# Performance work log

Measured on AMD Instinct MI355X. Metric: run time of the kernel, lower is better.

## Reference

```python
import jax, jax.numpy as jnp
import numpy as np

B, S, D, H, DK, HID = 2, 2048, 768, 12, 64, 3072
EPS = 1e-5

def layernorm(x, g, b):
    mu = jnp.mean(x, axis=-1, keepdims=True)
    var = jnp.var(x, axis=-1, keepdims=True)
    return (x - mu) * jax.lax.rsqrt(var + EPS) * g + b

def setup_inputs() -> dict:
    key = jax.random.key(0)
    ks = jax.random.split(key, 9)
    std = 0.02
    x = jax.random.normal(ks[0], (B, S, D), dtype=jnp.float32)
    Wq = jax.random.normal(ks[1], (H, D, DK), dtype=jnp.float32) * std
    Wk = jax.random.normal(ks[2], (H, D, DK), dtype=jnp.float32) * std
    Wv = jax.random.normal(ks[3], (H, D, DK), dtype=jnp.float32) * std
    Wo = jax.random.normal(ks[4], (H * DK, D), dtype=jnp.float32) * std
    W1 = jax.random.normal(ks[5], (D, HID), dtype=jnp.float32) * std
    b1 = jnp.zeros((HID,), dtype=jnp.float32)
    W2 = jax.random.normal(ks[6], (HID, D), dtype=jnp.float32) * std
    b2 = jnp.zeros((D,), dtype=jnp.float32)
    g_ln1 = jnp.ones((D,), dtype=jnp.float32)
    b_ln1 = jnp.zeros((D,), dtype=jnp.float32)
    g_ln2 = jnp.ones((D,), dtype=jnp.float32)
    b_ln2 = jnp.zeros((D,), dtype=jnp.float32)
    return {"x": x, "Wq": Wq, "Wk": Wk, "Wv": Wv, "Wo": Wo,
            "W1": W1, "b1": b1, "W2": W2, "b2": b2,
            "g_ln1": g_ln1, "b_ln1": b_ln1, "g_ln2": g_ln2, "b_ln2": b_ln2}

def reference(x, Wq, Wk, Wv, Wo, W1, b1, W2, b2, g_ln1, b_ln1, g_ln2, b_ln2):
    seq = x.shape[1]
    h = layernorm(x, g_ln1, b_ln1)
    # per-head projections, vectorized over heads: [B,H,S,DK]
    Q = jnp.einsum('bsd,hdk->bhsk', h, Wq)
    K = jnp.einsum('bsd,hdk->bhsk', h, Wk)
    V = jnp.einsum('bsd,hdk->bhsk', h, Wv)
    scores = jnp.einsum('bhsk,bhtk->bhst', Q, K) / jnp.sqrt(jnp.float32(DK))
    mask = jnp.triu(jnp.full((seq, seq), -jnp.inf, dtype=scores.dtype), k=1)
    A = jax.nn.softmax(scores + mask, axis=-1)
    out = jnp.einsum('bhst,bhtk->bhsk', A, V)  # [B,H,S,DK]
    # concat heads (matches torch.cat over heads dim=-1)
    out = out.transpose(0, 2, 1, 3).reshape(x.shape[0], seq, H * DK)
    attn = out @ Wo
    y = x + attn
    h2 = layernorm(y, g_ln2, b_ln2)
    mlp = jax.nn.gelu(h2 @ W1 + b1, approximate=False) @ W2 + b2
    return y + mlp
```

## Files before the change

kernel.cpp:

```cpp
#include <hip/hip_runtime.h>
#include <hip/hip_bf16.h>
#include <cstdint>
#include <cstddef>

using bf16 = __hip_bfloat16;
typedef __attribute__((ext_vector_type(8))) short short8;
typedef __attribute__((ext_vector_type(4))) float f32x4;
typedef __attribute__((ext_vector_type(2))) int i32x2;

#define DEV static __device__ __forceinline__

#define MROWS 4096
#define SEQ   2048
#define DMODEL 768
#define NHEAD 12
#define DHEAD 64
#define HID   3072
#define QSCALE 0.1803368801111204f

DEV void gload16(const void* g, void* l) {
  __builtin_amdgcn_global_load_lds((const __attribute__((address_space(1))) void*)g,
                                   (__attribute__((address_space(3))) void*)l, 16, 0, 0);
}

template <int CTRL>
DEV float dppf(float x) {
  return __builtin_bit_cast(float,
      __builtin_amdgcn_mov_dpp(__builtin_bit_cast(int, x), CTRL, 0xF, 0xF, true));
}
DEV float red_add16(float x) {
  x += dppf<0xB1>(x);
  x += dppf<0x4E>(x);
  x += dppf<0x141>(x);
  x += dppf<0x140>(x);
  return x;
}

DEV float gelu_exact(float x) {
  float z = fabsf(x) * 0.70710678118f;
  float t = __builtin_amdgcn_rcpf(fmaf(0.3275911f, z, 1.0f));
  float poly = fmaf(1.061405429f, t, -1.453152027f);
  poly = fmaf(poly, t, 1.421413741f);
  poly = fmaf(poly, t, -0.284496736f);
  poly = fmaf(poly, t, 0.254829592f);
  poly *= t;
  float e = __builtin_amdgcn_exp2f(-0.72134752044f * x * x);
  float erfv = fmaf(-poly, e, 1.0f);
  erfv = copysignf(erfv, x);
  return 0.5f * x * (1.0f + erfv);
}

__global__ __launch_bounds__(256) void cvt_qkv_k(const float* __restrict__ Wq,
                                                 const float* __restrict__ Wk,
                                                 const float* __restrict__ Wv,
                                                 bf16* __restrict__ out) {
  int idx = blockIdx.x * 256 + threadIdx.x;
  int n = idx / DMODEL, d = idx - n * DMODEL;
  int proj = n / DMODEL;
  int within = n - proj * DMODEL;
  int hh = within >> 6, k = within & 63;
  const float* W = (proj == 0) ? Wq : (proj == 1 ? Wk : Wv);
  out[idx] = __float2bfloat16(W[((size_t)hh * DMODEL + d) * DHEAD + k]);
}

__global__ __launch_bounds__(256) void cvt_t_k(const float* __restrict__ W,
                                               bf16* __restrict__ out, int R, int C) {
  int idx = blockIdx.x * 256 + threadIdx.x;
  int c = idx / R, r = idx - c * R;
  out[idx] = __float2bfloat16(W[(size_t)r * C + c]);
}

__global__ __launch_bounds__(256) void ln_k(const float* __restrict__ in,
                                            const float* __restrict__ gam,
                                            const float* __restrict__ bet,
                                            bf16* __restrict__ out) {
  int r = blockIdx.x;
  int tid = threadIdx.x;
  const float* p = in + (size_t)r * DMODEL;
  float v0 = p[tid], v1 = p[tid + 256], v2 = p[tid + 512];
  float s = v0 + v1 + v2;
  float ss = v0 * v0 + v1 * v1 + v2 * v2;
#pragma unroll
  for (int off = 1; off < 64; off <<= 1) {
    s += __shfl_xor(s, off);
    ss += __shfl_xor(ss, off);
  }
  __shared__ float rs[4], rss[4];
  int w = tid >> 6, l = tid & 63;
  if (l == 0) { rs[w] = s; rss[w] = ss; }
  __syncthreads();
  s = rs[0] + rs[1] + rs[2] + rs[3];
  ss = rss[0] + rss[1] + rss[2] + rss[3];
  float mean = s * (1.0f / 768.0f);
  float var = ss * (1.0f / 768.0f) - mean * mean;
  float inv = rsqrtf(var + 1e-5f);
  bf16* o = out + (size_t)r * DMODEL;
  o[tid]       = __float2bfloat16((v0 - mean) * inv * gam[tid] + bet[tid]);
  o[tid + 256] = __float2bfloat16((v1 - mean) * inv * gam[tid + 256] + bet[tid + 256]);
  o[tid + 512] = __float2bfloat16((v2 - mean) * inv * gam[tid + 512] + bet[tid + 512]);
}

template <int EPI>
DEV void gemm_epilogue(int r, int c, float v,
                       bf16* __restrict__ ob, float* __restrict__ of,
                       const float* __restrict__ add, const float* __restrict__ bias,
                       bf16* __restrict__ vt) {
  if constexpr (EPI == 0) {
    if (c < 1536) {
      float scv = (c < DMODEL) ? QSCALE : 1.0f;
      ob[(size_t)r * 1536 + c] = __float2bfloat16(v * scv);
    } else {
      int within = c - 1536;
      int hh = within >> 6, kk = within & 63;
      int bidx = r >> 11, sq = r & 2047;
      int sqp = (sq & ~63) | ((sq & 15) << 2) | ((sq >> 4) & 3);
      vt[(((size_t)bidx * NHEAD + hh) * DHEAD + kk) * SEQ + sqp] = __float2bfloat16(v);
    }
  } else if constexpr (EPI == 1) {
    of[(size_t)r * DMODEL + c] = add[(size_t)r * DMODEL + c] + v;
  } else if constexpr (EPI == 2) {
    ob[(size_t)r * HID + c] = __float2bfloat16(gelu_exact(v + bias[c]));
  } else {
    of[(size_t)r * DMODEL + c] = add[(size_t)r * DMODEL + c] + v + bias[c];
  }
}

template <int EPI, int BM, int BN>
__global__ __launch_bounds__(256) void gemm_bt(const bf16* __restrict__ A,
                                               const bf16* __restrict__ Bt, int K,
                                               bf16* __restrict__ ob,
                                               float* __restrict__ of,
                                               const float* __restrict__ add,
                                               const float* __restrict__ bias,
                                               bf16* __restrict__ vt) {
  __shared__ bf16 sA[2][BM * 32];
  __shared__ bf16 sB[2][BN * 32];
  constexpr int MI = BM / 32;
  constexpr int NI = BN / 32;
  constexpr int LOADS = (BM == 128 ? 2 : 1) + (BN == 128 ? 2 : 1);
  const int tid = threadIdx.x;
  const int w = tid >> 6, l = tid & 63;
  const int lr = l & 15, lg = l >> 4;
  const int mbase = blockIdx.y * BM, nbase = blockIdx.x * BN;
  const int wm = (w >> 1) * (BM / 2), wn = (w & 1) * (BN / 2);

  f32x4 acc[MI][NI];
#pragma unroll
  for (int i = 0; i < MI; ++i)
#pragma unroll
    for (int j = 0; j < NI; ++j) acc[i][j] = (f32x4)0.0f;

  const int srow = l >> 2;
  const int scol = ((l & 3) ^ ((l >> 3) & 3)) * 8;
  const bf16* gA = A + (size_t)(mbase + (BM == 128 ? w * 32 : w * 16) + srow) * K + scol;
  const bf16* gB = Bt + (size_t)(nbase + (BN == 128 ? w * 32 : w * 16) + srow) * K + scol;
  const int foff = (lg ^ ((lr >> 1) & 3)) * 8;

#define GSTAGE(bufi, t)                                                      \
  {                                                                          \
    const int k0_ = (t) * 32;                                                \
    if constexpr (BM == 128) {                                               \
      gload16(gA + k0_, &sA[bufi][w * 1024]);                                \
      gload16(gA + k0_ + (size_t)16 * K, &sA[bufi][w * 1024 + 512]);         \
    } else {                                                                 \
      gload16(gA + k0_, &sA[bufi][w * 512]);                                 \
    }                                                                        \
    if constexpr (BN == 128) {                                               \
      gload16(gB + k0_, &sB[bufi][w * 1024]);                                \
      gload16(gB + k0_ + (size_t)16 * K, &sB[bufi][w * 1024 + 512]);         \
    } else {                                                                 \
      gload16(gB + k0_, &sB[bufi][w * 512]);                                 \
    }                                                                        \
  }

  const int nt = K >> 5;
  GSTAGE(0, 0);
  for (int t = 0; t < nt; ++t) {
    const int cur = t & 1;
    if (t + 1 < nt) {
      GSTAGE(cur ^ 1, t + 1);
      if constexpr (LOADS == 4)      asm volatile("s_waitcnt vmcnt(4)" ::: "memory");
      else if constexpr (LOADS == 3) asm volatile("s_waitcnt vmcnt(3)" ::: "memory");
      else                           asm volatile("s_waitcnt vmcnt(2)" ::: "memory");
    } else {
      asm volatile("s_waitcnt vmcnt(0)" ::: "memory");
    }
    __builtin_amdgcn_s_barrier();

    short8 a[MI], bb[NI];
#pragma unroll
    for (int mi = 0; mi < MI; ++mi)
      a[mi] = *(const short8*)&sA[cur][(wm + mi * 16 + lr) * 32 + foff];
#pragma unroll
    for (int ni = 0; ni < NI; ++ni)
      bb[ni] = *(const short8*)&sB[cur][(wn + ni * 16 + lr) * 32 + foff];
#pragma unroll
    for (int mi = 0; mi < MI; ++mi)
#pragma unroll
      for (int ni = 0; ni < NI; ++ni)
        acc[mi][ni] = __builtin_amdgcn_mfma_f32_16x16x32_bf16(a[mi], bb[ni], acc[mi][ni], 0, 0, 0);

    __builtin_amdgcn_s_barrier();
  }
#undef GSTAGE

  const int row0 = mbase + wm + lg * 4;
  const int col0 = nbase + wn + lr;
#pragma unroll
  for (int mi = 0; mi < MI; ++mi)
#pragma unroll
    for (int ni = 0; ni < NI; ++ni)
#pragma unroll
      for (int i = 0; i < 4; ++i)
        gemm_epilogue<EPI>(row0 + mi * 16 + i, col0 + ni * 16, acc[mi][ni][i],
                           ob, of, add, bias, vt);
}

template <int EPI>
__global__ __launch_bounds__(256) void gemm64_bt(const bf16* __restrict__ A,
                                                 const bf16* __restrict__ Bt, int K,
                                                 bf16* __restrict__ ob,
                                                 float* __restrict__ of,
                                                 const float* __restrict__ add,
                                                 const float* __restrict__ bias) {
  __shared__ bf16 sA[2][64 * 64];
  __shared__ bf16 sB[2][64 * 64];
  const int tid = threadIdx.x;
  const int w = tid >> 6, l = tid & 63;
  const int lr = l & 15, lg = l >> 4;
  const int mbase = blockIdx.y * 64, nbase = blockIdx.x * 64;
  const int wm = (w >> 1) * 32, wn = (w & 1) * 32;

  f32x4 acc[2][2];
#pragma unroll
  for (int i = 0; i < 2; ++i)
#pragma unroll
    for (int j = 0; j < 2; ++j) acc[i][j] = (f32x4)0.0f;

  const int srow3 = l >> 3;
  const int csrc = ((l & 7) ^ srow3) * 8;
  const bf16* gA = A + (size_t)(mbase + w * 16 + srow3) * K + csrc;
  const bf16* gB = Bt + (size_t)(nbase + w * 16 + srow3) * K + csrc;

  int rowa[2], rowb[2], cswz[2];
#pragma unroll
  for (int mi = 0; mi < 2; ++mi) rowa[mi] = (wm + mi * 16 + lr) * 64;
#pragma unroll
  for (int ni = 0; ni < 2; ++ni) rowb[ni] = (wn + ni * 16 + lr) * 64;
#pragma unroll
  for (int kk = 0; kk < 2; ++kk) cswz[kk] = (((kk * 4 + lg) ^ (lr & 7)) << 3);

#define GSTAGE64(bufi, t)                                                    \
  {                                                                          \
    const int k0_ = (t) * 64;                                                \
    gload16(gA + k0_,                 &sA[bufi][(w * 16) * 64]);             \
    gload16(gA + k0_ + (size_t)8 * K, &sA[bufi][(w * 16 + 8) * 64]);         \
    gload16(gB + k0_,                 &sB[bufi][(w * 16) * 64]);             \
    gload16(gB + k0_ + (size_t)8 * K, &sB[bufi][(w * 16 + 8) * 64]);         \
  }

  const int nt = K >> 6;
  GSTAGE64(0, 0);
  for (int t = 0; t < nt; ++t) {
    const int cur = t & 1;
    if (t + 1 < nt) {
      GSTAGE64(cur ^ 1, t + 1);
      asm volatile("s_waitcnt vmcnt(4)" ::: "memory");
    } else {
      asm volatile("s_waitcnt vmcnt(0)" ::: "memory");
    }
    __builtin_amdgcn_s_barrier();

    short8 a[2][2], bb[2][2];
#pragma unroll
    for (int mi = 0; mi < 2; ++mi)
#pragma unroll
      for (int kk = 0; kk < 2; ++kk)
        a[mi][kk] = *(const short8*)&sA[cur][rowa[mi] + cswz[kk]];
#pragma unroll
    for (int ni = 0; ni < 2; ++ni)
#pragma unroll
      for (int kk = 0; kk < 2; ++kk)
        bb[ni][kk] = *(const short8*)&sB[cur][rowb[ni] + cswz[kk]];
#pragma unroll
    for (int mi = 0; mi < 2; ++mi)
#pragma unroll
      for (int ni = 0; ni < 2; ++ni) {
        acc[mi][ni] = __builtin_amdgcn_mfma_f32_16x16x32_bf16(a[mi][0], bb[ni][0], acc[mi][ni], 0, 0, 0);
        acc[mi][ni] = __builtin_amdgcn_mfma_f32_16x16x32_bf16(a[mi][1], bb[ni][1], acc[mi][ni], 0, 0, 0);
      }

    __builtin_amdgcn_s_barrier();
  }
#undef GSTAGE64

  const int row0 = mbase + wm + lg * 4;
  const int col0 = nbase + wn + lr;
#pragma unroll
  for (int mi = 0; mi < 2; ++mi)
#pragma unroll
    for (int ni = 0; ni < 2; ++ni)
#pragma unroll
      for (int i = 0; i < 4; ++i)
        gemm_epilogue<EPI>(row0 + mi * 16 + i, col0 + ni * 16, acc[mi][ni][i],
                           ob, of, add, bias, nullptr);
}

__global__ __launch_bounds__(256) void attn_k(const bf16* __restrict__ qk,
                                              const bf16* __restrict__ vt,
                                              bf16* __restrict__ o,
                                              float* __restrict__ opart,
                                              float* __restrict__ lpart) {
  __shared__ bf16 sK[2][64 * 64];
  __shared__ bf16 sV[2][64 * 64];
  __shared__ bf16 sP[64 * 64];

  const int d = blockIdx.x;
  const int bh = d % 24;
  const int rank = d / 24;
  const int j = 79 - rank;
  int qt, chunk, nch;
  if (j < 8)       { qt = j;                        chunk = 0;           nch = 1; }
  else if (j < 24) { int r_ = j - 8;  qt = 8  + (r_ >> 1); chunk = r_ & 1;  nch = 2; }
  else if (j < 48) { int r_ = j - 24; qt = 16 + r_ / 3;    chunk = r_ % 3;  nch = 3; }
  else             { int r_ = j - 48; qt = 24 + (r_ >> 2); chunk = r_ & 3;  nch = 4; }
  const int nt_q = qt + 1;
  const int t0 = (chunk * nt_q) / nch;
  const int t1 = ((chunk + 1) * nt_q) / nch;

  const int b = bh / NHEAD, h = bh - b * NHEAD;
  const int qbase = qt * 64;
  const int tid = threadIdx.x, w = tid >> 6, l = tid & 63;
  const int lr = l & 15, lg = l >> 4;

  short8 q[2];
#pragma unroll
  for (int kk = 0; kk < 2; ++kk)
    q[kk] = *(const short8*)&qk[(size_t)(b * SEQ + qbase + w * 16 + lr) * 1536 + h * DHEAD + kk * 32 + lg * 8];

  f32x4 oa[4];
  float lst[4];
#pragma unroll
  for (int i = 0; i < 4; ++i) { oa[i] = (f32x4)0.0f; lst[i] = 0.0f; }

  const int srow3 = l >> 3;
  const int csrc = (l & 7) ^ srow3;
  const bf16* gKb = qk + ((size_t)(b * SEQ) + w * 16 + srow3) * 1536 + DMODEL + h * DHEAD + csrc * 8;
  const bf16* gVb = vt + ((size_t)bh * DHEAD + w * 16 + srow3) * SEQ + csrc * 8;

  int rowb[4], cswz[2];
#pragma unroll
  for (int ni = 0; ni < 4; ++ni) rowb[ni] = (ni * 16 + lr) * 64;
#pragma unroll
  for (int kk = 0; kk < 2; ++kk) cswz[kk] = (((kk * 4 + lg) ^ (lr & 7)) << 3);
  const int prow = (w * 16 + lr) * 64;

#define STAGE(buf, t)                                                              \
  {                                                                                \
    const int kb_ = (t) * 64;                                                      \
    gload16(gKb + (size_t)kb_ * 1536,        &sK[buf][(w * 16) * 64]);             \
    gload16(gKb + (size_t)(kb_ + 8) * 1536,  &sK[buf][(w * 16 + 8) * 64]);         \
    gload16(gVb + kb_,                       &sV[buf][(w * 16) * 64]);             \
    gload16(gVb + kb_ + (size_t)8 * SEQ,     &sV[buf][(w * 16 + 8) * 64]);         \
  }

  STAGE(0, t0);

  for (int t = t0; t < t1; ++t) {
    const int cur = (t - t0) & 1;
    const int kb = t * 64;
    if (t + 1 < t1) {
      STAGE(cur ^ 1, t + 1);
      asm volatile("s_waitcnt vmcnt(4)" ::: "memory");
    } else {
      asm volatile("s_waitcnt vmcnt(0)" ::: "memory");
    }
    __builtin_amdgcn_s_barrier();

    const bf16* sKc = sK[cur];
    const bf16* sVc = sV[cur];

    f32x4 sc[4];
    __builtin_amdgcn_s_setprio(1);
#pragma unroll
    for (int ni = 0; ni < 4; ++ni) {
      sc[ni] = (f32x4)0.0f;
#pragma unroll
      for (int kk = 0; kk < 2; ++kk) {
        short8 kf = *(const short8*)&sKc[rowb[ni] + cswz[kk]];
        sc[ni] = __builtin_amdgcn_mfma_f32_16x16x32_bf16(q[kk], kf, sc[ni], 0, 0, 0);
      }
    }
    __builtin_amdgcn_s_setprio(0);

    const bool need_mask = (kb + 63) > (qbase + w * 16);
    const int qrow0 = qbase + w * 16 + lg * 4;
#pragma unroll
    for (int i = 0; i < 4; ++i) {
      float v0 = sc[0][i], v1 = sc[1][i], v2 = sc[2][i], v3 = sc[3][i];
      if (need_mask) {
        const int qg = qrow0 + i;
        v0 = (kb + lr      > qg) ? -1e30f : v0;
        v1 = (kb + 16 + lr > qg) ? -1e30f : v1;
        v2 = (kb + 32 + lr > qg) ? -1e30f : v2;
        v3 = (kb + 48 + lr > qg) ? -1e30f : v3;
      }
      float p0 = exp2f(v0), p1 = exp2f(v1), p2 = exp2f(v2), p3 = exp2f(v3);
      lst[i] += (p0 + p1) + (p2 + p3);
      int r0, r1;
      asm("v_cvt_pk_bf16_f32 %0, %1, %2" : "=v"(r0) : "v"(p0), "v"(p1));
      asm("v_cvt_pk_bf16_f32 %0, %1, %2" : "=v"(r1) : "v"(p2), "v"(p3));
      const int rrow = w * 16 + lg * 4 + i;
      *(i32x2*)((char*)sP + rrow * 128 + ((lr * 8) ^ ((rrow & 7) << 4))) = (i32x2){r0, r1};
    }

    short8 pf0 = *(const short8*)&sP[prow + cswz[0]];
    short8 pf1 = *(const short8*)&sP[prow + cswz[1]];
    __builtin_amdgcn_s_setprio(1);
#pragma unroll
    for (int nk = 0; nk < 4; ++nk) {
      short8 vf0 = *(const short8*)&sVc[rowb[nk] + cswz[0]];
      short8 vf1 = *(const short8*)&sVc[rowb[nk] + cswz[1]];
      oa[nk] = __builtin_amdgcn_mfma_f32_16x16x32_bf16(pf0, vf0, oa[nk], 0, 0, 0);
      oa[nk] = __builtin_amdgcn_mfma_f32_16x16x32_bf16(pf1, vf1, oa[nk], 0, 0, 0);
    }
    __builtin_amdgcn_s_setprio(0);
    __builtin_amdgcn_s_barrier();
  }
#undef STAGE

#pragma unroll
  for (int i = 0; i < 4; ++i) lst[i] = red_add16(lst[i]);

  if (nch == 1) {
#pragma unroll
    for (int i = 0; i < 4; ++i) {
      const float rl = __builtin_amdgcn_rcpf(lst[i]);
#pragma unroll
      for (int nk = 0; nk < 4; ++nk) {
        int row = qbase + w * 16 + lg * 4 + i;
        int col = h * DHEAD + nk * 16 + lr;
        o[(size_t)(b * SEQ + row) * DMODEL + col] = __float2bfloat16(oa[nk][i] * rl);
      }
    }
  } else {
    const int slot = bh * 80 + j;
    float* op = opart + (size_t)slot * 4096;
#pragma unroll
    for (int i = 0; i < 4; ++i) {
      const int row = w * 16 + lg * 4 + i;
#pragma unroll
      for (int nk = 0; nk < 4; ++nk)
        op[row * 64 + nk * 16 + lr] = oa[nk][i];
      if (lr == 0) lpart[slot * 64 + row] = lst[i];
    }
  }
}

__global__ __launch_bounds__(256) void attn_comb_k(const float* __restrict__ opart,
                                                   const float* __restrict__ lpart,
                                                   bf16* __restrict__ o) {
  const int s = blockIdx.x;
  const int bh = s / 24;
  const int qt = 8 + (s - bh * 24);
  const int b = bh / NHEAD, h = bh - b * NHEAD;
  const int bb = qt >> 3;
  const int nch = bb + 1;
  const int S0 = 4 * bb * (bb + 1) + (qt - 8 * bb) * (bb + 1);
  const int slot0 = bh * 80 + S0;

  const int tid = threadIdx.x;
  const int row = tid >> 2;
  const int c0 = (tid & 3) * 16;

  f32x4 acc[4];
#pragma unroll
  for (int e = 0; e < 4; ++e) acc[e] = (f32x4)0.0f;
  float lsum = 0.0f;
  for (int c = 0; c < nch; ++c) {
    const f32x4* op = (const f32x4*)(opart + (size_t)(slot0 + c) * 4096 + row * 64 + c0);
    lsum += lpart[(slot0 + c) * 64 + row];
#pragma unroll
    for (int e = 0; e < 4; ++e) acc[e] += op[e];
  }
  const float rl = 1.0f / lsum;
  bf16* po = o + (size_t)(b * SEQ + qt * 64 + row) * DMODEL + h * DHEAD + c0;
#pragma unroll
  for (int e = 0; e < 4; ++e)
#pragma unroll
    for (int k = 0; k < 4; ++k)
      po[e * 4 + k] = __float2bfloat16(acc[e][k] * rl);
}

extern "C" void kernel_launch(void* const* d_in, const int* in_sizes, int n_in,
                              void* d_out, int out_size, void* d_ws, size_t ws_size,
                              hipStream_t stream) {
  (void)in_sizes; (void)n_in; (void)out_size; (void)ws_size;
  const float* x   = (const float*)d_in[0];
  const float* Wq  = (const float*)d_in[1];
  const float* Wk  = (const float*)d_in[2];
  const float* Wv  = (const float*)d_in[3];
  const float* Wo  = (const float*)d_in[4];
  const float* W1  = (const float*)d_in[5];
  const float* b1  = (const float*)d_in[6];
  const float* W2  = (const float*)d_in[7];
  const float* b2  = (const float*)d_in[8];
  const float* g1  = (const float*)d_in[9];
  const float* be1 = (const float*)d_in[10];
  const float* g2  = (const float*)d_in[11];
  const float* be2 = (const float*)d_in[12];
  float* out = (float*)d_out;

  char* p = (char*)d_ws;
  bf16* WqkvT = (bf16*)p; p += (size_t)2304 * 768 * 2;
  bf16* WoT   = (bf16*)p; p += (size_t)768 * 768 * 2;
  bf16* W1T   = (bf16*)p; p += (size_t)3072 * 768 * 2;
  bf16* W2T   = (bf16*)p; p += (size_t)768 * 3072 * 2;
  bf16* h1    = (bf16*)p; p += (size_t)MROWS * DMODEL * 2;
  char* alias0 = p;
  bf16* QK    = (bf16*)p; p += (size_t)MROWS * 1536 * 2;
  bf16* Vt    = (bf16*)p; p += (size_t)24 * DHEAD * SEQ * 2;
  bf16* O     = (bf16*)p; p += (size_t)MROWS * DMODEL * 2;
  float* y    = (float*)p; p += (size_t)MROWS * DMODEL * 4;
  bf16* h2    = (bf16*)p; p += (size_t)MROWS * DMODEL * 2;
  float* Opart = (float*)p; p += (size_t)24 * 80 * 4096 * 4;
  float* Lpart = (float*)p; p += (size_t)24 * 80 * 64 * 4;
  bf16* U     = (bf16*)alias0;

  dim3 blk(256);
  cvt_qkv_k<<<(2304 * 768) / 256, blk, 0, stream>>>(Wq, Wk, Wv, WqkvT);
  cvt_t_k<<<(768 * 768) / 256, blk, 0, stream>>>(Wo, WoT, 768, 768);
  cvt_t_k<<<(768 * 3072) / 256, blk, 0, stream>>>(W1, W1T, 768, 3072);
  cvt_t_k<<<(3072 * 768) / 256, blk, 0, stream>>>(W2, W2T, 3072, 768);
  ln_k<<<MROWS, blk, 0, stream>>>(x, g1, be1, h1);
  gemm_bt<0, 128, 128><<<dim3(18, 32), blk, 0, stream>>>(h1, WqkvT, 768, QK, nullptr, nullptr, nullptr, Vt);
  attn_k<<<1920, blk, 0, stream>>>(QK, Vt, O, Opart, Lpart);
  attn_comb_k<<<576, blk, 0, stream>>>(Opart, Lpart, O);
  gemm64_bt<1><<<dim3(12, 64), blk, 0, stream>>>(O, WoT, 768, nullptr, y, x, nullptr);
  ln_k<<<MROWS, blk, 0, stream>>>(y, g2, be2, h2);
  gemm64_bt<2><<<dim3(48, 64), blk, 0, stream>>>(h2, W1T, 768, U, nullptr, nullptr, b1);
  gemm64_bt<3><<<dim3(12, 64), blk, 0, stream>>>(U, W2T, 3072, nullptr, out, y, b2);
}
```

Baseline: 218.8 us.

## Use LDS-tiled transpose for weight conversion and 64x64 GEMM for QKV

Replaces the naive strided-read weight transpose-and-convert kernels with 64x64 shared-memory tiled transposes. Both the reads and the bf16 writes become coalesced. The QKV projection moves from the 128x128 GEMM to the 64x64 K-step-64 GEMM, giving 2304 blocks instead of 576 for better CU occupancy. The cost is less operand reuse per block in the QKV GEMM.

```diff
diff --git a/kernel.cpp b/kernel.cpp
--- a/kernel.cpp
+++ b/kernel.cpp
@@ -50,24 +50,46 @@
   return 0.5f * x * (1.0f + erfv);
 }
 
-__global__ __launch_bounds__(256) void cvt_qkv_k(const float* __restrict__ Wq,
-                                                 const float* __restrict__ Wk,
-                                                 const float* __restrict__ Wv,
-                                                 bf16* __restrict__ out) {
-  int idx = blockIdx.x * 256 + threadIdx.x;
-  int n = idx / DMODEL, d = idx - n * DMODEL;
-  int proj = n / DMODEL;
-  int within = n - proj * DMODEL;
-  int hh = within >> 6, k = within & 63;
-  const float* W = (proj == 0) ? Wq : (proj == 1 ? Wk : Wv);
-  out[idx] = __float2bfloat16(W[((size_t)hh * DMODEL + d) * DHEAD + k]);
-}
-
-__global__ __launch_bounds__(256) void cvt_t_k(const float* __restrict__ W,
-                                               bf16* __restrict__ out, int R, int C) {
-  int idx = blockIdx.x * 256 + threadIdx.x;
-  int c = idx / R, r = idx - c * R;
-  out[idx] = __float2bfloat16(W[(size_t)r * C + c]);
+__global__ __launch_bounds__(256) void tcvt_k(const float* __restrict__ in,
+                                              bf16* __restrict__ out, int R, int C) {
+  __shared__ float tile[64][65];
+  const int r0 = blockIdx.y * 64, c0 = blockIdx.x * 64;
+  const int tid = threadIdx.x, lr = tid & 63, lw = tid >> 6;
+#pragma unroll
+  for (int i = 0; i < 16; ++i) {
+    int r = i * 4 + lw;
+    tile[r][lr] = in[(size_t)(r0 + r) * C + c0 + lr];
+  }
+  __syncthreads();
+#pragma unroll
+  for (int i = 0; i < 16; ++i) {
+    int c = i * 4 + lw;
+    out[(size_t)(c0 + c) * R + r0 + lr] = __float2bfloat16(tile[lr][c]);
+  }
+}
+
+__global__ __launch_bounds__(256) void tcvt_qkv_k(const float* __restrict__ Wq,
+                                                  const float* __restrict__ Wk,
+                                                  const float* __restrict__ Wv,
+                                                  bf16* __restrict__ out) {
+  __shared__ float tile[64][65];
+  const int z = blockIdx.z;
+  const int proj = z / 12, hh = z - proj * 12;
+  const float* W = (proj == 0 ? Wq : (proj == 1 ? Wk : Wv)) + (size_t)hh * DMODEL * DHEAD;
+  bf16* o = out + (size_t)(proj * DMODEL + hh * DHEAD) * DMODEL;
+  const int r0 = blockIdx.y * 64;
+  const int tid = threadIdx.x, lr = tid & 63, lw = tid >> 6;
+#pragma unroll
+  for (int i = 0; i < 16; ++i) {
+    int r = i * 4 + lw;
+    tile[r][lr] = W[(size_t)(r0 + r) * DHEAD + lr];
+  }
+  __syncthreads();
+#pragma unroll
+  for (int i = 0; i < 16; ++i) {
+    int c = i * 4 + lw;
+    o[(size_t)c * DMODEL + r0 + lr] = __float2bfloat16(tile[lr][c]);
+  }
 }
 
 __global__ __launch_bounds__(256) void ln_k(const float* __restrict__ in,
@@ -125,104 +147,14 @@
   }
 }
 
-template <int EPI, int BM, int BN>
-__global__ __launch_bounds__(256) void gemm_bt(const bf16* __restrict__ A,
-                                               const bf16* __restrict__ Bt, int K,
-                                               bf16* __restrict__ ob,
-                                               float* __restrict__ of,
-                                               const float* __restrict__ add,
-                                               const float* __restrict__ bias,
-                                               bf16* __restrict__ vt) {
-  __shared__ bf16 sA[2][BM * 32];
-  __shared__ bf16 sB[2][BN * 32];
-  constexpr int MI = BM / 32;
-  constexpr int NI = BN / 32;
-  constexpr int LOADS = (BM == 128 ? 2 : 1) + (BN == 128 ? 2 : 1);
-  const int tid = threadIdx.x;
-  const int w = tid >> 6, l = tid & 63;
-  const int lr = l & 15, lg = l >> 4;
-  const int mbase = blockIdx.y * BM, nbase = blockIdx.x * BN;
-  const int wm = (w >> 1) * (BM / 2), wn = (w & 1) * (BN / 2);
-
-  f32x4 acc[MI][NI];
-#pragma unroll
-  for (int i = 0; i < MI; ++i)
-#pragma unroll
-    for (int j = 0; j < NI; ++j) acc[i][j] = (f32x4)0.0f;
-
-  const int srow = l >> 2;
-  const int scol = ((l & 3) ^ ((l >> 3) & 3)) * 8;
-  const bf16* gA = A + (size_t)(mbase + (BM == 128 ? w * 32 : w * 16) + srow) * K + scol;
-  const bf16* gB = Bt + (size_t)(nbase + (BN == 128 ? w * 32 : w * 16) + srow) * K + scol;
-  const int foff = (lg ^ ((lr >> 1) & 3)) * 8;
-
-#define GSTAGE(bufi, t)                                                      \
-  {                                                                          \
-    const int k0_ = (t) * 32;                                                \
-    if constexpr (BM == 128) {                                               \
-      gload16(gA + k0_, &sA[bufi][w * 1024]);                                \
-      gload16(gA + k0_ + (size_t)16 * K, &sA[bufi][w * 1024 + 512]);         \
-    } else {                                                                 \
-      gload16(gA + k0_, &sA[bufi][w * 512]);                                 \
-    }                                                                        \
-    if constexpr (BN == 128) {                                               \
-      gload16(gB + k0_, &sB[bufi][w * 1024]);                                \
-      gload16(gB + k0_ + (size_t)16 * K, &sB[bufi][w * 1024 + 512]);         \
-    } else {                                                                 \
-      gload16(gB + k0_, &sB[bufi][w * 512]);                                 \
-    }                                                                        \
-  }
-
-  const int nt = K >> 5;
-  GSTAGE(0, 0);
-  for (int t = 0; t < nt; ++t) {
-    const int cur = t & 1;
-    if (t + 1 < nt) {
-      GSTAGE(cur ^ 1, t + 1);
-      if constexpr (LOADS == 4)      asm volatile("s_waitcnt vmcnt(4)" ::: "memory");
-      else if constexpr (LOADS == 3) asm volatile("s_waitcnt vmcnt(3)" ::: "memory");
-      else                           asm volatile("s_waitcnt vmcnt(2)" ::: "memory");
-    } else {
-      asm volatile("s_waitcnt vmcnt(0)" ::: "memory");
-    }
-    __builtin_amdgcn_s_barrier();
-
-    short8 a[MI], bb[NI];
-#pragma unroll
-    for (int mi = 0; mi < MI; ++mi)
-      a[mi] = *(const short8*)&sA[cur][(wm + mi * 16 + lr) * 32 + foff];
-#pragma unroll
-    for (int ni = 0; ni < NI; ++ni)
-      bb[ni] = *(const short8*)&sB[cur][(wn + ni * 16 + lr) * 32 + foff];
-#pragma unroll
-    for (int mi = 0; mi < MI; ++mi)
-#pragma unroll
-      for (int ni = 0; ni < NI; ++ni)
-        acc[mi][ni] = __builtin_amdgcn_mfma_f32_16x16x32_bf16(a[mi], bb[ni], acc[mi][ni], 0, 0, 0);
-
-    __builtin_amdgcn_s_barrier();
-  }
-#undef GSTAGE
-
-  const int row0 = mbase + wm + lg * 4;
-  const int col0 = nbase + wn + lr;
-#pragma unroll
-  for (int mi = 0; mi < MI; ++mi)
-#pragma unroll
-    for (int ni = 0; ni < NI; ++ni)
-#pragma unroll
-      for (int i = 0; i < 4; ++i)
-        gemm_epilogue<EPI>(row0 + mi * 16 + i, col0 + ni * 16, acc[mi][ni][i],
-                           ob, of, add, bias, vt);
-}
-
 template <int EPI>
 __global__ __launch_bounds__(256) void gemm64_bt(const bf16* __restrict__ A,
                                                  const bf16* __restrict__ Bt, int K,
                                                  bf16* __restrict__ ob,
                                                  float* __restrict__ of,
                                                  const float* __restrict__ add,
-                                                 const float* __restrict__ bias) {
+                                                 const float* __restrict__ bias,
+                                                 bf16* __restrict__ vt) {
   __shared__ bf16 sA[2][64 * 64];
   __shared__ bf16 sB[2][64 * 64];
   const int tid = threadIdx.x;
@@ -303,7 +235,7 @@
 #pragma unroll
       for (int i = 0; i < 4; ++i)
         gemm_epilogue<EPI>(row0 + mi * 16 + i, col0 + ni * 16, acc[mi][ni][i],
-                           ob, of, add, bias, nullptr);
+                           ob, of, add, bias, vt);
 }
 
 __global__ __launch_bounds__(256) void attn_k(const bf16* __restrict__ qk,
@@ -528,16 +460,16 @@
   bf16* U     = (bf16*)alias0;
 
   dim3 blk(256);
-  cvt_qkv_k<<<(2304 * 768) / 256, blk, 0, stream>>>(Wq, Wk, Wv, WqkvT);
-  cvt_t_k<<<(768 * 768) / 256, blk, 0, stream>>>(Wo, WoT, 768, 768);
-  cvt_t_k<<<(768 * 3072) / 256, blk, 0, stream>>>(W1, W1T, 768, 3072);
-  cvt_t_k<<<(3072 * 768) / 256, blk, 0, stream>>>(W2, W2T, 3072, 768);
+  tcvt_qkv_k<<<dim3(1, 12, 36), blk, 0, stream>>>(Wq, Wk, Wv, WqkvT);
+  tcvt_k<<<dim3(12, 12), blk, 0, stream>>>(Wo, WoT, 768, 768);
+  tcvt_k<<<dim3(48, 12), blk, 0, stream>>>(W1, W1T, 768, 3072);
+  tcvt_k<<<dim3(12, 48), blk, 0, stream>>>(W2, W2T, 3072, 768);
   ln_k<<<MROWS, blk, 0, stream>>>(x, g1, be1, h1);
-  gemm_bt<0, 128, 128><<<dim3(18, 32), blk, 0, stream>>>(h1, WqkvT, 768, QK, nullptr, nullptr, nullptr, Vt);
+  gemm64_bt<0><<<dim3(36, 64), blk, 0, stream>>>(h1, WqkvT, 768, QK, nullptr, nullptr, nullptr, Vt);
   attn_k<<<1920, blk, 0, stream>>>(QK, Vt, O, Opart, Lpart);
   attn_comb_k<<<576, blk, 0, stream>>>(Opart, Lpart, O);
-  gemm64_bt<1><<<dim3(12, 64), blk, 0, stream>>>(O, WoT, 768, nullptr, y, x, nullptr);
+  gemm64_bt<1><<<dim3(12, 64), blk, 0, stream>>>(O, WoT, 768, nullptr, y, x, nullptr, nullptr);
   ln_k<<<MROWS, blk, 0, stream>>>(y, g2, be2, h2);
-  gemm64_bt<2><<<dim3(48, 64), blk, 0, stream>>>(h2, W1T, 768, U, nullptr, nullptr, b1);
-  gemm64_bt<3><<<dim3(12, 64), blk, 0, stream>>>(U, W2T, 3072, nullptr, out, y, b2);
-}
+  gemm64_bt<2><<<dim3(48, 64), blk, 0, stream>>>(h2, W1T, 768, U, nullptr, nullptr, b1, nullptr);
+  gemm64_bt<3><<<dim3(12, 64), blk, 0, stream>>>(U, W2T, 3072, nullptr, out, y, b2, nullptr);
+}
```

Result: faster. 188.9 us (-13.6%).
